# Kernel tuning notes

Hardware: AMD Instinct MI355X
Metric: run time of the kernel (lower is better)

## Reference

```python
import jax, jax.numpy as jnp
import numpy as np

N, E, B = 131072, 262144, 4096
NODE_DIM, EDGE_DIM, HIDDEN = 16, 4, 64
MLP_HID = 128


def setup_inputs() -> dict:
    key = jax.random.key(0)
    ks = jax.random.split(key, 16)
    def nrm(k, shape, s=0.05):
        return jax.random.normal(k, shape, jnp.float32) * s
    return {
        "x": jax.random.normal(ks[0], (N, NODE_DIM), jnp.float32),
        "edge_attr": jax.random.normal(ks[1], (E, EDGE_DIM), jnp.float32),
        "edge_index": jax.random.randint(ks[2], (2, E), 0, N),
        "batch": jnp.sort(jax.random.randint(ks[3], (N,), 0, B)),
        "w_e1": nrm(ks[4], (EDGE_DIM, MLP_HID)),
        "b_e1": jnp.zeros((MLP_HID,), jnp.float32),
        "w_e2": nrm(ks[5], (MLP_HID, NODE_DIM * HIDDEN)),
        "b_e2": jnp.zeros((NODE_DIM * HIDDEN,), jnp.float32),
        "root": nrm(ks[6], (NODE_DIM, HIDDEN)),
        "conv_bias": jnp.zeros((HIDDEN,), jnp.float32),
        "gru_wih": nrm(ks[7], (3 * HIDDEN, HIDDEN)),
        "gru_whh": nrm(ks[8], (3 * HIDDEN, HIDDEN)),
        "gru_bih": jnp.zeros((3 * HIDDEN,), jnp.float32),
        "gru_bhh": jnp.zeros((3 * HIDDEN,), jnp.float32),
        "lstm_wih": nrm(ks[9], (4 * HIDDEN, 2 * HIDDEN)),
        "lstm_whh": nrm(ks[10], (4 * HIDDEN, HIDDEN)),
        "lstm_bih": jnp.zeros((4 * HIDDEN,), jnp.float32),
        "lstm_bhh": jnp.zeros((4 * HIDDEN,), jnp.float32),
        "fc1_w": nrm(ks[11], (2 * HIDDEN, HIDDEN)),
        "fc1_b": jnp.zeros((HIDDEN,), jnp.float32),
        "fc2_w": nrm(ks[12], (HIDDEN, 1)),
        "fc2_b": jnp.zeros((1,), jnp.float32),
    }


def reference(x, edge_attr, edge_index, batch,
              w_e1, b_e1, w_e2, b_e2, root, conv_bias,
              gru_wih, gru_whh, gru_bih, gru_bhh,
              lstm_wih, lstm_whh, lstm_bih, lstm_bhh,
              fc1_w, fc1_b, fc2_w, fc2_b):
    src, dst = edge_index[0], edge_index[1]
    # NNConv: edge-MLP -> per-edge weight [E, node_dim, hidden]
    Wdyn = (jax.nn.relu(edge_attr @ w_e1 + b_e1) @ w_e2 + b_e2).reshape(E, NODE_DIM, HIDDEN)
    msg = jnp.einsum('ed,edh->eh', x[src], Wdyn)  # gather + per-edge matmul
    msum = jax.ops.segment_sum(msg, dst, num_segments=N)
    cnt = jax.ops.segment_sum(jnp.ones((E,), msg.dtype), dst, num_segments=N)
    agg = msum / jnp.maximum(cnt, 1.0)[:, None]  # scatter-mean
    out = jax.nn.relu(agg + x @ root + conv_bias)
    h = out
    for _ in range(3):
        gi = out @ gru_wih.T + gru_bih
        gh = h @ gru_whh.T + gru_bhh
        ir, iz, inn = jnp.split(gi, 3, axis=-1)
        hr, hz, hn = jnp.split(gh, 3, axis=-1)
        r = jax.nn.sigmoid(ir + hr)
        z = jax.nn.sigmoid(iz + hz)
        n = jnp.tanh(inn + r * hn)
        h = (1.0 - z) * n + z * h
        out = h
    # Set2Set, 3 processing steps
    hl = jnp.zeros((B, HIDDEN), out.dtype)
    cl = jnp.zeros((B, HIDDEN), out.dtype)
    q_star = jnp.zeros((B, 2 * HIDDEN), out.dtype)
    for _ in range(3):
        gates = q_star @ lstm_wih.T + lstm_bih + hl @ lstm_whh.T + lstm_bhh
        ig, fg, gg, og = jnp.split(gates, 4, axis=-1)
        ig = jax.nn.sigmoid(ig); fg = jax.nn.sigmoid(fg)
        gg = jnp.tanh(gg); og = jax.nn.sigmoid(og)
        cl = fg * cl + ig * gg
        hl = og * jnp.tanh(cl)
        q = hl  # [B, H]
        e = jnp.sum(out * q[batch], axis=-1)  # [N]
        m = jax.lax.stop_gradient(jax.ops.segment_max(e, batch, num_segments=B))
        ex = jnp.exp(e - m[batch])
        denom = jax.ops.segment_sum(ex, batch, num_segments=B)
        a = ex / denom[batch]  # segment softmax
        r_g = jax.ops.segment_sum(a[:, None] * out, batch, num_segments=B)
        q_star = jnp.concatenate([q, r_g], axis=-1)
    y = jax.nn.relu(q_star @ fc1_w + fc1_b)
    return (y @ fc2_w + fc2_b).squeeze(-1)
```

## Files before the change

### kernel.cpp

```cpp
#include <hip/hip_runtime.h>
#include <math.h>

#define N_NODES 131072
#define N_EDGES 262144
#define N_B     4096

typedef __attribute__((ext_vector_type(8))) short short8;
typedef __attribute__((ext_vector_type(8))) _Float16 half8;
typedef __attribute__((ext_vector_type(4))) float f32x4;
typedef __attribute__((ext_vector_type(16))) float f32x16;

__device__ __forceinline__ float fast_sig(float x) {
    return 1.0f / (1.0f + __expf(-x));
}
__device__ __forceinline__ float fast_tanh(float x) {
    float t = __expf(-2.0f * fabsf(x));
    float r = (1.0f - t) / (1.0f + t);
    return copysignf(r, x);
}

__device__ __forceinline__ void split_fp16(float v, _Float16& hi, _Float16& lo) {
    _Float16 h = (_Float16)v;
    hi = h;
    lo = (_Float16)(v - (float)h);
}

__global__ __launch_bounds__(256) void k_misc(
    const float* __restrict__ we2, unsigned short* __restrict__ wt,
    const float* __restrict__ gwih, const float* __restrict__ gwhh,
    const float* __restrict__ gbih, const float* __restrict__ gbhh,
    unsigned short* __restrict__ wtg, float* __restrict__ gbias,
    const float* __restrict__ lwih, const float* __restrict__ lwhh,
    float4* __restrict__ wA, float4* __restrict__ wB,
    const int* __restrict__ batch, int* __restrict__ starts,
    const int* __restrict__ eidx, int* __restrict__ deg)
{
    const int bid = blockIdx.x;
    const int tid = threadIdx.x;
    if (bid >= 105) {
        int p = (bid - 105) * 256 + tid;
        atomicAdd(&deg[eidx[N_EDGES + p]], 1);
        return;
    }
    if (bid < 64) {
        int p = bid * 256 + tid;
        int d = p >> 10;
        int u = (p >> 9) & 1;
        int s = (p >> 6) & 7;
        int l = p & 63;
        int k0 = s * 16 + ((l >> 5) << 3);
        int h = u * 32 + (l & 31);
        half8 hv;
        #pragma unroll
        for (int j = 0; j < 8; ++j) {
            float v = we2[(size_t)(k0 + j) * 1024 + d * 64 + h];
            hv[j] = (_Float16)v;
        }
        size_t base = (size_t)d * 8192 + (size_t)u * 4096 + s * 512 + l * 8;
        *(half8*)&wt[base] = hv;
    } else if (bid < 72) {
        int p = (bid - 64) * 256 + tid;
        if (p < 256) {
            int g = p >> 6, j = p & 63;
            float b;
            if (g == 0)      b = gbih[j] + gbhh[j];
            else if (g == 1) b = gbih[64 + j] + gbhh[64 + j];
            else if (g == 2) b = gbih[128 + j];
            else             b = gbhh[128 + j];
            gbias[p] = b;
        }
        int u = p >> 7, ks = (p >> 6) & 1, ln = p & 63;
        int n = u * 16 + (ln & 15);
        int g = n >> 6, jn = n & 63;
        int k0 = ks * 32 + (ln >> 4) * 8;
        half8 hv;
        #pragma unroll
        for (int jj = 0; jj < 8; ++jj) {
            int k = k0 + jj;
            float v;
            if (g == 0)      v = gwih[jn * 64 + k] + gwhh[jn * 64 + k];
            else if (g == 1) v = gwih[(64 + jn) * 64 + k] + gwhh[(64 + jn) * 64 + k];
            else if (g == 2) v = gwih[(128 + jn) * 64 + k];
            else             v = gwhh[(128 + jn) * 64 + k];
            hv[jj] = (_Float16)v;
        }
        size_t base = (size_t)(u * 2 + ks) * 512 + ln * 8;
        *(half8*)&wtg[base] = hv;
    } else if (bid < 88) {
        int p = (bid - 72) * 256 + tid;
        int k = p >> 6, ln = p & 63;
        float4 a, b;
        a.x = lwih[(0 * 64 + ln) * 128 + k] + lwhh[(0 * 64 + ln) * 64 + k];
        a.y = lwih[(1 * 64 + ln) * 128 + k] + lwhh[(1 * 64 + ln) * 64 + k];
        a.z = lwih[(2 * 64 + ln) * 128 + k] + lwhh[(2 * 64 + ln) * 64 + k];
        a.w = lwih[(3 * 64 + ln) * 128 + k] + lwhh[(3 * 64 + ln) * 64 + k];
        b.x = lwih[(0 * 64 + ln) * 128 + 64 + k];
        b.y = lwih[(1 * 64 + ln) * 128 + 64 + k];
        b.z = lwih[(2 * 64 + ln) * 128 + 64 + k];
        b.w = lwih[(3 * 64 + ln) * 128 + 64 + k];
        wA[p] = a; wB[p] = b;
    } else {
        int g = (bid - 88) * 256 + tid;
        if (g > N_B) return;
        if (g == N_B) { starts[N_B] = N_NODES; return; }
        int lo = 0, hi = N_NODES;
        while (lo < hi) {
            int mid = (lo + hi) >> 1;
            if (batch[mid] < g) lo = mid + 1; else hi = mid;
        }
        starts[g] = lo;
    }
}

__global__ __launch_bounds__(256) void k_scan1(
    const int* __restrict__ deg, int* __restrict__ psum)
{
    __shared__ int sm[256];
    const int t = threadIdx.x;
    sm[t] = deg[blockIdx.x * 256 + t];
    __syncthreads();
    #pragma unroll
    for (int off = 128; off; off >>= 1) {
        if (t < off) sm[t] += sm[t + off];
        __syncthreads();
    }
    if (t == 0) psum[blockIdx.x] = sm[0];
}

__global__ __launch_bounds__(512) void k_scan2(
    const int* __restrict__ psum, int* __restrict__ psumx)
{
    __shared__ int sm[512];
    const int t = threadIdx.x;
    sm[t] = psum[t];
    __syncthreads();
    #pragma unroll
    for (int off = 1; off < 512; off <<= 1) {
        int add = (t >= off) ? sm[t - off] : 0;
        __syncthreads();
        sm[t] += add;
        __syncthreads();
    }
    psumx[t] = (t > 0) ? sm[t - 1] : 0;
}

__global__ __launch_bounds__(256) void k_scan3(
    const int* __restrict__ deg, const int* __restrict__ psumx,
    int* __restrict__ row_ptr, int* __restrict__ cursor)
{
    __shared__ int sm[256];
    const int t = threadIdx.x;
    const int i = blockIdx.x * 256 + t;
    int d = deg[i];
    sm[t] = d;
    __syncthreads();
    #pragma unroll
    for (int off = 1; off < 256; off <<= 1) {
        int add = (t >= off) ? sm[t - off] : 0;
        __syncthreads();
        sm[t] += add;
        __syncthreads();
    }
    int excl = sm[t] - d + psumx[blockIdx.x];
    row_ptr[i] = excl;
    cursor[i] = excl;
    if (i == 0) row_ptr[N_NODES] = N_EDGES;
}

__global__ __launch_bounds__(256) void k_scat(
    const int* __restrict__ eidx, int* __restrict__ cursor,
    int* __restrict__ eord)
{
    int e = blockIdx.x * 256 + threadIdx.x;
    int dst = eidx[N_EDGES + e];
    int pos = atomicAdd(&cursor[dst], 1);
    eord[pos] = e;
}

__global__ __launch_bounds__(256)
__attribute__((amdgpu_waves_per_eu(3, 4)))
void k_edge(
    const float* __restrict__ x,
    const float* __restrict__ ea,
    const int*   __restrict__ eidx,
    const float* __restrict__ we1,
    const float* __restrict__ be1,
    const unsigned short* __restrict__ wt,
    const float* __restrict__ be2,
    float* __restrict__ emsg)
{
    __shared__ unsigned short sAh[16384];
    __shared__ float sxT[16 * 136];
    __shared__ float sbe2[1024];

    const int tid = threadIdx.x;
    const int w   = tid >> 6;
    const int ln  = tid & 63;
    const int u     = w >> 1;
    const int mbase = (w & 1) * 2;
    const int eb  = blockIdx.x * 128;

    #pragma unroll
    for (int v = tid; v < 1024; v += 256) sbe2[v] = be2[v];

    #pragma unroll
    for (int v = tid; v < 512; v += 256) {
        int e = v >> 2, q = v & 3;
        int src = eidx[eb + e];
        float4 t4 = ((const float4*)(x + (size_t)src * 16))[q];
        sxT[(q * 4 + 0) * 136 + e] = t4.x;
        sxT[(q * 4 + 1) * 136 + e] = t4.y;
        sxT[(q * 4 + 2) * 136 + e] = t4.z;
        sxT[(q * 4 + 3) * 136 + e] = t4.w;
    }

    #pragma unroll 1
    for (int i = 0; i < 8; ++i) {
        int cc = tid + i * 256;
        int mt = cc >> 9;
        int s  = (cc >> 6) & 7;
        int l  = cc & 63;
        int e   = mt * 32 + (l & 31);
        int kk0 = s * 16 + ((l >> 5) << 3);
        float4 eav = *(const float4*)(ea + (size_t)(eb + e) * 4);
        float4 b0 = *(const float4*)(be1 + kk0);
        float4 b1 = *(const float4*)(be1 + kk0 + 4);
        float acc[8] = {b0.x, b0.y, b0.z, b0.w, b1.x, b1.y, b1.z, b1.w};
        #pragma unroll
        for (int a = 0; a < 4; ++a) {
            float4 wa0 = *(const float4*)(we1 + a * 128 + kk0);
            float4 wa1 = *(const float4*)(we1 + a * 128 + kk0 + 4);
            float ev = (a == 0) ? eav.x : (a == 1) ? eav.y : (a == 2) ? eav.z : eav.w;
            acc[0] += ev * wa0.x; acc[1] += ev * wa0.y;
            acc[2] += ev * wa0.z; acc[3] += ev * wa0.w;
            acc[4] += ev * wa1.x; acc[5] += ev * wa1.y;
            acc[6] += ev * wa1.z; acc[7] += ev * wa1.w;
        }
        half8 hv;
        #pragma unroll
        for (int j = 0; j < 8; ++j) {
            hv[j] = (_Float16)fmaxf(acc[j], 0.0f);
        }
        *(half8*)&sAh[cc * 8] = hv;
    }
    __syncthreads();

    half8 ah[2][8];
    #pragma unroll
    for (int m2 = 0; m2 < 2; ++m2) {
        int mt = mbase + m2;
        #pragma unroll
        for (int s = 0; s < 8; ++s) {
            ah[m2][s] = *(half8*)&sAh[((mt * 8 + s) * 64 + ln) * 8];
        }
    }
    #pragma unroll
    for (int m2 = 0; m2 < 2; ++m2) {
        #pragma unroll
        for (int s = 0; s < 8; ++s) {
            asm volatile("" : "+v"(ah[m2][s]));
        }
    }

    const unsigned short* wdu = wt + (size_t)u * 4096;
    const int d0 = blockIdx.x & 15;
    const int rbase = (ln >> 5) * 4;

    f32x16 msg[2];
    #pragma unroll
    for (int r = 0; r < 16; ++r) { msg[0][r] = 0.0f; msg[1][r] = 0.0f; }

    half8 bq[8];
    {
        const unsigned short* p0 = wdu + (size_t)d0 * 8192 + ln * 8;
        #pragma unroll
        for (int f = 0; f < 7; ++f) bq[f] = *(const half8*)(p0 + f * 512);
    }

    #pragma unroll 1
    for (int dd = 0; dd < 16; ++dd) {
        const int d = (d0 + dd) & 15;
        const unsigned short* wd  = wdu + (size_t)d * 8192;
        const unsigned short* wnx = wdu + (size_t)((d + 1) & 15) * 8192;

        float bv = sbe2[d * 64 + u * 32 + (ln & 31)];
        f32x16 c2[2];
        #pragma unroll
        for (int r = 0; r < 16; ++r) { c2[0][r] = bv; c2[1][r] = bv; }

        #pragma unroll
        for (int s = 0; s < 8; ++s) {
            if (s == 0) {
                bq[7] = *(const half8*)(wd + 7 * 512 + ln * 8);
            } else if (dd < 15) {
                bq[s - 1] = *(const half8*)(wnx + (s - 1) * 512 + ln * 8);
            }
            half8 bb = bq[s];
            c2[0] = __builtin_amdgcn_mfma_f32_32x32x16_f16(ah[0][s], bb, c2[0], 0, 0, 0);
            c2[1] = __builtin_amdgcn_mfma_f32_32x32x16_f16(ah[1][s], bb, c2[1], 0, 0, 0);
        }
        #pragma unroll
        for (int m2 = 0; m2 < 2; ++m2) {
            #pragma unroll
            for (int q = 0; q < 4; ++q) {
                f32x4 xv = *(const f32x4*)&sxT[d * 136 + (mbase + m2) * 32 + rbase + 8 * q];
                #pragma unroll
                for (int j = 0; j < 4; ++j) {
                    msg[m2][q * 4 + j] = fmaf(xv[j], c2[m2][q * 4 + j], msg[m2][q * 4 + j]);
                }
            }
        }
    }

    const int col = u * 32 + (ln & 31);
    #pragma unroll
    for (int m2 = 0; m2 < 2; ++m2) {
        #pragma unroll
        for (int r = 0; r < 16; ++r) {
            int row = (r & 3) + ((r >> 2) * 8) + rbase;
            emsg[(size_t)(eb + (mbase + m2) * 32 + row) * 64 + col] = msg[m2][r];
        }
    }
}

__global__ __launch_bounds__(256, 2) void k_gru2(
    float* __restrict__ buf,
    const float* __restrict__ emsg,
    const int* __restrict__ rowp,
    const int* __restrict__ eord,
    const float* __restrict__ x,
    const float* __restrict__ root,
    const float* __restrict__ cb,
    const unsigned short* __restrict__ wtg,
    const float* __restrict__ gbias)
{
    __shared__ unsigned short sAh[16384];
    __shared__ unsigned short sAl[16384];
    __shared__ float sroot[1024];
    __shared__ float sbias[256];
    __shared__ float scb[64];
    const int tid = threadIdx.x;
    const int w = tid >> 6, ln = tid & 63, lq = ln >> 4, lm = ln & 15;
    const size_t nbase = (size_t)blockIdx.x * 256;

    #pragma unroll
    for (int v = tid; v < 1024; v += 256) sroot[v] = root[v];
    sbias[tid] = gbias[tid];
    if (tid < 64) scb[tid] = cb[tid];
    __syncthreads();

    #pragma unroll 2
    for (int i = 0; i < 8; ++i) {
        int cc = tid + i * 256;
        int mt = cc >> 7, ks = (cc >> 6) & 1, l = cc & 63;
        size_t gn = nbase + mt * 16 + (l & 15);
        int c0 = ks * 32 + (l >> 4) * 8;
        int rp0 = rowp[gn], rp1 = rowp[gn + 1];
        float ms[8] = {0.f, 0.f, 0.f, 0.f, 0.f, 0.f, 0.f, 0.f};
        for (int k = rp0; k < rp1; ++k) {
            int e = eord[k];
            float4 m0 = *(const float4*)(emsg + (size_t)e * 64 + c0);
            float4 m1 = *(const float4*)(emsg + (size_t)e * 64 + c0 + 4);
            ms[0] += m0.x; ms[1] += m0.y; ms[2] += m0.z; ms[3] += m0.w;
            ms[4] += m1.x; ms[5] += m1.y; ms[6] += m1.z; ms[7] += m1.w;
        }
        float cinv = 1.0f / fmaxf((float)(rp1 - rp0), 1.0f);
        float xv[16];
        *(float4*)&xv[0]  = *(const float4*)(x + gn * 16);
        *(float4*)&xv[4]  = *(const float4*)(x + gn * 16 + 4);
        *(float4*)&xv[8]  = *(const float4*)(x + gn * 16 + 8);
        *(float4*)&xv[12] = *(const float4*)(x + gn * 16 + 12);
        float acc[8];
        #pragma unroll
        for (int j = 0; j < 8; ++j) acc[j] = scb[c0 + j];
        #pragma unroll
        for (int d = 0; d < 16; ++d) {
            float xd = xv[d];
            #pragma unroll
            for (int j = 0; j < 8; ++j) acc[j] += xd * sroot[d * 64 + c0 + j];
        }
        half8 hv, lv;
        #pragma unroll
        for (int j = 0; j < 8; ++j) {
            float hval = fmaxf(ms[j] * cinv + acc[j], 0.0f);
            _Float16 hi, lo; split_fp16(hval, hi, lo);
            hv[j] = hi; lv[j] = lo;
        }
        *(half8*)&sAh[cc * 8] = hv;
        *(half8*)&sAl[cc * 8] = lv;
    }
    __syncthreads();

    float hreg[4][4][4];
    #pragma unroll 1
    for (int step = 0; step < 3; ++step) {
        half8 ah[4][2], al[4][2];
        #pragma unroll
        for (int i = 0; i < 4; ++i)
            #pragma unroll
            for (int ks = 0; ks < 2; ++ks) {
                int mt = w * 4 + i;
                ah[i][ks] = *(half8*)&sAh[((mt * 2 + ks) * 64 + ln) * 8];
                al[i][ks] = *(half8*)&sAl[((mt * 2 + ks) * 64 + ln) * 8];
            }
        if (step == 0) {
            #pragma unroll
            for (int v = 0; v < 4; ++v) {
                int ksp = v >> 1;
                int lq2 = (v & 1) * 2 + (lm >> 3);
                int jp = lm & 7;
                #pragma unroll
                for (int i = 0; i < 4; ++i) {
                    int mt = w * 4 + i;
                    #pragma unroll
                    for (int r = 0; r < 4; ++r) {
                        int idx = ((mt * 2 + ksp) * 64 + lq2 * 16 + lq * 4 + r) * 8 + jp;
                        float hi = (float)*(const _Float16*)&sAh[idx];
                        float lo = (float)*(const _Float16*)&sAl[idx];
                        hreg[v][i][r] = hi + lo;
                    }
                }
            }
        }
        __syncthreads();

        #pragma unroll 1
        for (int v = 0; v < 4; ++v) {
            f32x4 C[4][4];
            #pragma unroll
            for (int g = 0; g < 4; ++g) {
                float bv = sbias[g * 64 + v * 16 + lm];
                #pragma unroll
                for (int i = 0; i < 4; ++i) C[g][i] = (f32x4){bv, bv, bv, bv};
            }
            #pragma unroll
            for (int g = 0; g < 4; ++g) {
                int u = g * 4 + v;
                #pragma unroll
                for (int ks = 0; ks < 2; ++ks) {
                    size_t wb = (size_t)(u * 2 + ks) * 512 + ln * 8;
                    half8 bb = *(const half8*)&wtg[wb];
                    #pragma unroll
                    for (int i = 0; i < 4; ++i) {
                        C[g][i] = __builtin_amdgcn_mfma_f32_16x16x32_f16(ah[i][ks], bb, C[g][i], 0, 0, 0);
                        C[g][i] = __builtin_amdgcn_mfma_f32_16x16x32_f16(al[i][ks], bb, C[g][i], 0, 0, 0);
                    }
                }
            }
            int ksp = v >> 1;
            int lq2 = (v & 1) * 2 + (lm >> 3);
            int jp = lm & 7;
            #pragma unroll
            for (int i = 0; i < 4; ++i) {
                int mt = w * 4 + i;
                #pragma unroll
                for (int r = 0; r < 4; ++r) {
                    float rr = fast_sig(C[0][i][r]);
                    float zz = fast_sig(C[1][i][r]);
                    float nn = fast_tanh(C[2][i][r] + rr * C[3][i][r]);
                    float hnew = (1.0f - zz) * nn + zz * hreg[v][i][r];
                    hreg[v][i][r] = hnew;
                    if (step < 2) {
                        _Float16 hi, lo; split_fp16(hnew, hi, lo);
                        int idx = ((mt * 2 + ksp) * 64 + lq2 * 16 + lq * 4 + r) * 8 + jp;
                        sAh[idx] = *(unsigned short*)&hi;
                        sAl[idx] = *(unsigned short*)&lo;
                    } else {
                        buf[(nbase + mt * 16 + lq * 4 + r) * 64 + v * 16 + lm] = hnew;
                    }
                }
            }
        }
        if (step < 2) __syncthreads();
    }
}

__global__ __launch_bounds__(256) void k_s2s(
    const float* __restrict__ out,
    const int*   __restrict__ starts,
    const float4* __restrict__ wA,
    const float4* __restrict__ wB,
    const float* __restrict__ bih,
    const float* __restrict__ bhh,
    const float* __restrict__ fc1w,
    const float* __restrict__ fc1b,
    const float* __restrict__ fc2w,
    const float* __restrict__ fc2b,
    float* __restrict__ y)
{
    __shared__ float osh[4][32][66];
    __shared__ float qsL[4][128];
    __shared__ float ebuf[4][256];
    const int tid = threadIdx.x;
    const int wv = tid >> 6, ln = tid & 63;
    const int gid = blockIdx.x * 4 + wv;

    const int s0 = starts[gid];
    int L = starts[gid + 1] - s0; if (L > 256) L = 256;
    const int SL = (L < 32) ? L : 32;

    #pragma unroll
    for (int base = 0; base < 32; base += 4) {
        int row = base + (ln >> 4);
        int c4 = (ln & 15) * 4;
        if (row < SL)
            *(float4*)&osh[wv][row][c4] =
                *(const float4*)(out + (size_t)(s0 + row) * 64 + c4);
    }

    qsL[wv][ln] = 0.0f; qsL[wv][64 + ln] = 0.0f;
    __builtin_amdgcn_wave_barrier();

    const float b0 = bih[ln] + bhh[ln];
    const float b1 = bih[64 + ln] + bhh[64 + ln];
    const float b2 = bih[128 + ln] + bhh[128 + ln];
    const float b3 = bih[192 + ln] + bhh[192 + ln];

    float c = 0.0f;

    #pragma unroll 1
    for (int step = 0; step < 3; ++step) {
        float a0 = b0, a1 = b1, a2 = b2, a3 = b3;
        #pragma unroll 4
        for (int k = 0; k < 64; ++k) {
            float qk = qsL[wv][k];
            float rk = qsL[wv][64 + k];
            float4 wa = wA[k * 64 + ln];
            float4 wb = wB[k * 64 + ln];
            a0 += wa.x * qk + wb.x * rk;
            a1 += wa.y * qk + wb.y * rk;
            a2 += wa.z * qk + wb.z * rk;
            a3 += wa.w * qk + wb.w * rk;
        }
        float ig = fast_sig(a0), fg = fast_sig(a1);
        float gg = fast_tanh(a2), og = fast_sig(a3);
        c = fg * c + ig * gg;
        float h = og * fast_tanh(c);
        __builtin_amdgcn_wave_barrier();
        qsL[wv][ln] = h;
        __builtin_amdgcn_wave_barrier();

        float m = -1e30f;
        for (int c0 = 0; c0 * 64 < L; ++c0) {
            int j = c0 * 64 + ln;
            if (j < L) {
                float a = 0.0f;
                if (j < SL) {
                    #pragma unroll
                    for (int l4 = 0; l4 < 16; ++l4) {
                        float4 ov = *(const float4*)&osh[wv][j][l4 * 4];
                        float4 hv = *(const float4*)&qsL[wv][l4 * 4];
                        a += ov.x * hv.x + ov.y * hv.y + ov.z * hv.z + ov.w * hv.w;
                    }
                } else {
                    const float4* orow = (const float4*)(out + (size_t)(s0 + j) * 64);
                    #pragma unroll
                    for (int l4 = 0; l4 < 16; ++l4) {
                        float4 ov = orow[l4];
                        float4 hv = *(const float4*)&qsL[wv][l4 * 4];
                        a += ov.x * hv.x + ov.y * hv.y + ov.z * hv.z + ov.w * hv.w;
                    }
                }
                ebuf[wv][j] = a;
                m = fmaxf(m, a);
            }
        }
        #pragma unroll
        for (int off = 32; off; off >>= 1) m = fmaxf(m, __shfl_xor(m, off));
        float ds = 0.0f;
        for (int c0 = 0; c0 * 64 < L; ++c0) {
            int j = c0 * 64 + ln;
            if (j < L) {
                float ex = __expf(ebuf[wv][j] - m);
                ebuf[wv][j] = ex;
                ds += ex;
            }
        }
        #pragma unroll
        for (int off = 32; off; off >>= 1) ds += __shfl_xor(ds, off);
        __builtin_amdgcn_wave_barrier();
        float rg = 0.0f;
        for (int j = 0; j < SL; ++j)
            rg = fmaf(ebuf[wv][j], osh[wv][j][ln], rg);
        for (int j = SL; j < L; ++j)
            rg = fmaf(ebuf[wv][j], out[(size_t)(s0 + j) * 64 + ln], rg);
        rg = (L > 0) ? (rg / ds) : 0.0f;
        qsL[wv][64 + ln] = rg;
        __builtin_amdgcn_wave_barrier();
    }

    float a = fc1b[ln];
    #pragma unroll 4
    for (int k = 0; k < 128; ++k)
        a = fmaf(qsL[wv][k], fc1w[k * 64 + ln], a);
    float uu = fmaxf(a, 0.0f) * fc2w[ln];
    #pragma unroll
    for (int off = 32; off; off >>= 1) uu += __shfl_xor(uu, off);
    if (ln == 0) y[gid] = uu + fc2b[0];
}

extern "C" void kernel_launch(void* const* d_in, const int* in_sizes, int n_in,
                              void* d_out, int out_size, void* d_ws, size_t ws_size,
                              hipStream_t stream) {
    const float* x     = (const float*)d_in[0];
    const float* ea    = (const float*)d_in[1];
    const int*   eidx  = (const int*)d_in[2];
    const int*   batch = (const int*)d_in[3];
    const float* we1   = (const float*)d_in[4];
    const float* be1   = (const float*)d_in[5];
    const float* we2   = (const float*)d_in[6];
    const float* be2   = (const float*)d_in[7];
    const float* root  = (const float*)d_in[8];
    const float* cb    = (const float*)d_in[9];
    const float* gwih  = (const float*)d_in[10];
    const float* gwhh  = (const float*)d_in[11];
    const float* gbih  = (const float*)d_in[12];
    const float* gbhh  = (const float*)d_in[13];
    const float* lwih  = (const float*)d_in[14];
    const float* lwhh  = (const float*)d_in[15];
    const float* lbih  = (const float*)d_in[16];
    const float* lbhh  = (const float*)d_in[17];
    const float* fc1w  = (const float*)d_in[18];
    const float* fc1b  = (const float*)d_in[19];
    const float* fc2w  = (const float*)d_in[20];
    const float* fc2b  = (const float*)d_in[21];

    float* emsg = (float*)d_ws;
    float* buf  = emsg + (size_t)N_EDGES * 64;
    int* deg    = (int*)(buf + (size_t)N_NODES * 64);
    int* rowp   = deg + N_NODES;
    int* cursor = rowp + N_NODES + 1;
    int* eord   = cursor + N_NODES;
    int* psum   = eord + N_EDGES;
    int* psumx  = psum + 512;
    int* starts = psumx + 512;
    size_t off = (size_t)((char*)(starts + N_B + 1) - (char*)d_ws);
    off = (off + 15) & ~(size_t)15;
    unsigned short* wt  = (unsigned short*)((char*)d_ws + off);
    unsigned short* wtg = wt + 262144;
    float* gbias = (float*)(wtg + 32768);
    float4* wA = (float4*)(gbias + 256);
    float4* wB = wA + 4096;
    float* y = (float*)d_out;

    hipMemsetAsync(deg, 0, (size_t)N_NODES * sizeof(int), stream);
    k_misc<<<1129, 256, 0, stream>>>(we2, wt, gwih, gwhh, gbih, gbhh, wtg, gbias,
                                     lwih, lwhh, wA, wB, batch, starts, eidx, deg);
    k_scan1<<<512, 256, 0, stream>>>(deg, psum);
    k_scan2<<<1, 512, 0, stream>>>(psum, psumx);
    k_scan3<<<512, 256, 0, stream>>>(deg, psumx, rowp, cursor);
    k_scat<<<1024, 256, 0, stream>>>(eidx, cursor, eord);
    k_edge<<<N_EDGES / 128, 256, 0, stream>>>(x, ea, eidx, we1, be1, wt, be2, emsg);
    k_gru2<<<N_NODES / 256, 256, 0, stream>>>(buf, emsg, rowp, eord, x, root, cb,
                                              wtg, gbias);
    k_s2s<<<N_B / 4, 256, 0, stream>>>(buf, starts, wA, wB, lbih, lbhh,
                                       fc1w, fc1b, fc2w, fc2b, y);
}
```

Baseline: 424.8 us.

## Fuse scatter-mean into edge kernel via atomics on dst-sorted edges

The edge kernel now handles edges in dst-sorted order (through eord) and atomically adds each message straight into a per-node sum buffer. This drops the 64 MB per-edge message array and the CSR gather loop in the GRU kernel, which now reads one summed row and divides by the degree. The cost is float atomics (sorting by destination lets neighbouring edges hit the same rows), indirect gathers of edge_attr and src, a larger memset, and summation order that is no longer deterministic.

```diff
diff --git a/kernel.cpp b/kernel.cpp
--- a/kernel.cpp
+++ b/kernel.cpp
@@ -146,7 +146,7 @@
 
 __global__ __launch_bounds__(256) void k_scan3(
     const int* __restrict__ deg, const int* __restrict__ psumx,
-    int* __restrict__ row_ptr, int* __restrict__ cursor)
+    int* __restrict__ cursor)
 {
     __shared__ int sm[256];
     const int t = threadIdx.x;
@@ -161,10 +161,7 @@
         sm[t] += add;
         __syncthreads();
     }
-    int excl = sm[t] - d + psumx[blockIdx.x];
-    row_ptr[i] = excl;
-    cursor[i] = excl;
-    if (i == 0) row_ptr[N_NODES] = N_EDGES;
+    cursor[i] = sm[t] - d + psumx[blockIdx.x];
 }
 
 __global__ __launch_bounds__(256) void k_scat(
@@ -183,15 +180,17 @@
     const float* __restrict__ x,
     const float* __restrict__ ea,
     const int*   __restrict__ eidx,
+    const int*   __restrict__ eord,
     const float* __restrict__ we1,
     const float* __restrict__ be1,
     const unsigned short* __restrict__ wt,
     const float* __restrict__ be2,
-    float* __restrict__ emsg)
+    float* __restrict__ msum)
 {
     __shared__ unsigned short sAh[16384];
     __shared__ float sxT[16 * 136];
     __shared__ float sbe2[1024];
+    __shared__ int   sdst[128];
 
     const int tid = threadIdx.x;
     const int w   = tid >> 6;
@@ -200,18 +199,23 @@
     const int mbase = (w & 1) * 2;
     const int eb  = blockIdx.x * 128;
 
+    if (tid < 128) {
+        int e = eord[eb + tid];
+        sdst[tid] = eidx[N_EDGES + e];
+    }
     #pragma unroll
     for (int v = tid; v < 1024; v += 256) sbe2[v] = be2[v];
 
     #pragma unroll
     for (int v = tid; v < 512; v += 256) {
-        int e = v >> 2, q = v & 3;
-        int src = eidx[eb + e];
+        int slot = v >> 2, q = v & 3;
+        int e = eord[eb + slot];
+        int src = eidx[e];
         float4 t4 = ((const float4*)(x + (size_t)src * 16))[q];
-        sxT[(q * 4 + 0) * 136 + e] = t4.x;
-        sxT[(q * 4 + 1) * 136 + e] = t4.y;
-        sxT[(q * 4 + 2) * 136 + e] = t4.z;
-        sxT[(q * 4 + 3) * 136 + e] = t4.w;
+        sxT[(q * 4 + 0) * 136 + slot] = t4.x;
+        sxT[(q * 4 + 1) * 136 + slot] = t4.y;
+        sxT[(q * 4 + 2) * 136 + slot] = t4.z;
+        sxT[(q * 4 + 3) * 136 + slot] = t4.w;
     }
 
     #pragma unroll 1
@@ -220,9 +224,10 @@
         int mt = cc >> 9;
         int s  = (cc >> 6) & 7;
         int l  = cc & 63;
-        int e   = mt * 32 + (l & 31);
-        int kk0 = s * 16 + ((l >> 5) << 3);
-        float4 eav = *(const float4*)(ea + (size_t)(eb + e) * 4);
+        int slot = mt * 32 + (l & 31);
+        int kk0  = s * 16 + ((l >> 5) << 3);
+        int ge = eord[eb + slot];
+        float4 eav = *(const float4*)(ea + (size_t)ge * 4);
         float4 b0 = *(const float4*)(be1 + kk0);
         float4 b1 = *(const float4*)(be1 + kk0 + 4);
         float acc[8] = {b0.x, b0.y, b0.z, b0.w, b1.x, b1.y, b1.z, b1.w};
@@ -318,16 +323,15 @@
         #pragma unroll
         for (int r = 0; r < 16; ++r) {
             int row = (r & 3) + ((r >> 2) * 8) + rbase;
-            emsg[(size_t)(eb + (mbase + m2) * 32 + row) * 64 + col] = msg[m2][r];
+            int dst = sdst[(mbase + m2) * 32 + row];
+            atomicAdd(msum + (size_t)dst * 64 + col, msg[m2][r]);
         }
     }
 }
 
 __global__ __launch_bounds__(256, 2) void k_gru2(
     float* __restrict__ buf,
-    const float* __restrict__ emsg,
-    const int* __restrict__ rowp,
-    const int* __restrict__ eord,
+    const int* __restrict__ deg,
     const float* __restrict__ x,
     const float* __restrict__ root,
     const float* __restrict__ cb,
@@ -349,22 +353,15 @@
     if (tid < 64) scb[tid] = cb[tid];
     __syncthreads();
 
-    #pragma unroll 2
+    #pragma unroll 1
     for (int i = 0; i < 8; ++i) {
         int cc = tid + i * 256;
         int mt = cc >> 7, ks = (cc >> 6) & 1, l = cc & 63;
         size_t gn = nbase + mt * 16 + (l & 15);
         int c0 = ks * 32 + (l >> 4) * 8;
-        int rp0 = rowp[gn], rp1 = rowp[gn + 1];
-        float ms[8] = {0.f, 0.f, 0.f, 0.f, 0.f, 0.f, 0.f, 0.f};
-        for (int k = rp0; k < rp1; ++k) {
-            int e = eord[k];
-            float4 m0 = *(const float4*)(emsg + (size_t)e * 64 + c0);
-            float4 m1 = *(const float4*)(emsg + (size_t)e * 64 + c0 + 4);
-            ms[0] += m0.x; ms[1] += m0.y; ms[2] += m0.z; ms[3] += m0.w;
-            ms[4] += m1.x; ms[5] += m1.y; ms[6] += m1.z; ms[7] += m1.w;
-        }
-        float cinv = 1.0f / fmaxf((float)(rp1 - rp0), 1.0f);
+        float4 m0 = *(const float4*)(buf + gn * 64 + c0);
+        float4 m1 = *(const float4*)(buf + gn * 64 + c0 + 4);
+        float cinv = 1.0f / fmaxf((float)deg[gn], 1.0f);
         float xv[16];
         *(float4*)&xv[0]  = *(const float4*)(x + gn * 16);
         *(float4*)&xv[4]  = *(const float4*)(x + gn * 16 + 4);
@@ -379,6 +376,7 @@
             #pragma unroll
             for (int j = 0; j < 8; ++j) acc[j] += xd * sroot[d * 64 + c0 + j];
         }
+        float ms[8] = {m0.x, m0.y, m0.z, m0.w, m1.x, m1.y, m1.z, m1.w};
         half8 hv, lv;
         #pragma unroll
         for (int j = 0; j < 8; ++j) {
@@ -625,11 +623,9 @@
     const float* fc2w  = (const float*)d_in[20];
     const float* fc2b  = (const float*)d_in[21];
 
-    float* emsg = (float*)d_ws;
-    float* buf  = emsg + (size_t)N_EDGES * 64;
+    float* buf  = (float*)d_ws;
     int* deg    = (int*)(buf + (size_t)N_NODES * 64);
-    int* rowp   = deg + N_NODES;
-    int* cursor = rowp + N_NODES + 1;
+    int* cursor = deg + N_NODES;
     int* eord   = cursor + N_NODES;
     int* psum   = eord + N_EDGES;
     int* psumx  = psum + 512;
@@ -643,16 +639,15 @@
     float4* wB = wA + 4096;
     float* y = (float*)d_out;
 
-    hipMemsetAsync(deg, 0, (size_t)N_NODES * sizeof(int), stream);
+    hipMemsetAsync(d_ws, 0, ((size_t)N_NODES * 64 + N_NODES) * sizeof(float), stream);
     k_misc<<<1129, 256, 0, stream>>>(we2, wt, gwih, gwhh, gbih, gbhh, wtg, gbias,
                                      lwih, lwhh, wA, wB, batch, starts, eidx, deg);
     k_scan1<<<512, 256, 0, stream>>>(deg, psum);
     k_scan2<<<1, 512, 0, stream>>>(psum, psumx);
-    k_scan3<<<512, 256, 0, stream>>>(deg, psumx, rowp, cursor);
+    k_scan3<<<512, 256, 0, stream>>>(deg, psumx, cursor);
     k_scat<<<1024, 256, 0, stream>>>(eidx, cursor, eord);
-    k_edge<<<N_EDGES / 128, 256, 0, stream>>>(x, ea, eidx, we1, be1, wt, be2, emsg);
-    k_gru2<<<N_NODES / 256, 256, 0, stream>>>(buf, emsg, rowp, eord, x, root, cb,
-                                              wtg, gbias);
+    k_edge<<<N_EDGES / 128, 256, 0, stream>>>(x, ea, eidx, eord, we1, be1, wt, be2, buf);
+    k_gru2<<<N_NODES / 256, 256, 0, stream>>>(buf, deg, x, root, cb, wtg, gbias);
     k_s2s<<<N_B / 4, 256, 0, stream>>>(buf, starts, wA, wB, lbih, lbhh,
                                        fc1w, fc1b, fc2w, fc2b, y);
 }
```

Result: slower. 443.1 us (+4.3%).
